# Performance work log

Measured on AMD Instinct MI355X. Metric: run time of the kernel, lower is better.

## Reference

```python
import jax, jax.numpy as jnp
from jax import lax
import numpy as np

L, D_LOCAL, BOND, BATCH = 64, 2, 64, 4096
STDDEV = 0.01  # default_kernel_init = normal(stddev=0.01)


def setup_inputs() -> dict:
    key = jax.random.key(0)
    k1, k2 = jax.random.split(key)
    x = jax.random.randint(k1, (BATCH, L), 0, D_LOCAL, dtype=jnp.int32)
    tensors_param = STDDEV * jax.random.normal(k2, (L, D_LOCAL, BOND, BOND), dtype=jnp.float32)
    return {"x": x, "tensors_param": tensors_param}


def reference(x, tensors_param):
    # tensors = param + identity (as in setup())
    P, d, D, _ = tensors_param.shape
    tensors = tensors_param + jnp.eye(D, dtype=tensors_param.dtype)  # [P, d, D, D]
    Lx = x.shape[-1]
    # tile unit cell across the chain (symperiod == L here, so tile factor is 1)
    all_tensors = jnp.tile(tensors, (Lx // P, 1, 1, 1))  # [L, d, D, D]
    B = x.shape[0]
    edge0 = jnp.broadcast_to(jnp.eye(D, dtype=tensors.dtype), (B, D, D))

    def step(edge, pair):
        t, qn = pair                      # t: [d, D, D], qn: [B]
        A = t[qn]                         # gather local matrices -> [B, D, D]
        return jnp.einsum('bij,bjk->bik', edge, A), None

    edge, _ = lax.scan(step, edge0, (all_tensors, x.T))  # scan over L sites
    psi = jnp.trace(edge, axis1=-2, axis2=-1)            # [B]
    return jnp.log(psi.astype(jnp.complex64))
```

## Files before the change

### kernel.cpp

```cpp
#include <hip/hip_runtime.h>


typedef __attribute__((ext_vector_type(8))) __bf16 bf16x8;
typedef __attribute__((ext_vector_type(4))) float f32x4;
typedef __attribute__((ext_vector_type(4))) int   int4v;

#define MFMA16(a, b, c) __builtin_amdgcn_mfma_f32_16x16x32_bf16((a), (b), (c), 0, 0, 0)

union frag_u { int4v i; bf16x8 v; };

__device__ __forceinline__ unsigned short f2bf(float f) {
  union { float f; unsigned u; } v; v.f = f;
  unsigned r = v.u + 0x7fffu + ((v.u >> 16) & 1u);
  return (unsigned short)(r >> 16);
}

__global__ __launch_bounds__(256) void prep_kernel(const float* __restrict__ p,
                                                   unsigned short* __restrict__ Tn,
                                                   unsigned short* __restrict__ Tt) {
  int t = blockIdx.x * 256 + threadIdx.x;
  int j  = t & 63;
  int i  = (t >> 6) & 63;
  int pq = t >> 12;
  float v = p[t] + ((i == j) ? 1.0f : 0.0f);
  unsigned short h = f2bf(v);
  Tn[t] = h;
  Tt[(((size_t)pq) << 12) + (size_t)j * 64 + i] = h;
}

__global__ __launch_bounds__(256) void build_p8_kernel(const unsigned short* __restrict__ Tn,
                                                       const unsigned short* __restrict__ Tt,
                                                       unsigned short* __restrict__ P8n,
                                                       unsigned short* __restrict__ P8t) {
  const int tid = threadIdx.x;
  const int l   = tid & 63;
  const int w   = blockIdx.x * 4 + (tid >> 6);
  const int s   = w >> 8, cmb = w & 255;
  const int c   = l & 15, p = l >> 4;

  const int srcA = (l & 15) | ((l & 16) << 1);
  const int srcB = srcA | 16;
  const bool hi5 = (l & 32) != 0;

  frag_u B[2][4];
  {
    int m7 = (8 * s + 7) * 2 + (cmb & 1);
    const unsigned short* base = Tt + ((size_t)m7 << 12);
#pragma unroll
    for (int ks = 0; ks < 2; ++ks)
#pragma unroll
      for (int nj = 0; nj < 4; ++nj)
        B[ks][nj].i = *reinterpret_cast<const int4v*>(base + (c + 16 * nj) * 64 + 32 * ks + 8 * p);
  }

#pragma unroll
  for (int j = 6; j >= 1; --j) {
    int m = (8 * s + j) * 2 + ((cmb >> (7 - j)) & 1);
    const unsigned short* abase = Tn + ((size_t)m << 12);
    frag_u A[4][2];
#pragma unroll
    for (int mi = 0; mi < 4; ++mi)
#pragma unroll
      for (int ks = 0; ks < 2; ++ks)
        A[mi][ks].i = *reinterpret_cast<const int4v*>(abase + (c + 16 * mi) * 64 + 32 * ks + 8 * p);

    int pk[4][4][2];
#pragma unroll
    for (int mi = 0; mi < 4; ++mi)
#pragma unroll
      for (int nj = 0; nj < 4; ++nj) {
        f32x4 d = {0.f, 0.f, 0.f, 0.f};
        d = MFMA16(A[mi][0].v, B[0][nj].v, d);
        d = MFMA16(A[mi][1].v, B[1][nj].v, d);
        asm("v_cvt_pk_bf16_f32 %0, %1, %2" : "=v"(pk[mi][nj][0]) : "v"(d[0]), "v"(d[1]));
        asm("v_cvt_pk_bf16_f32 %0, %1, %2" : "=v"(pk[mi][nj][1]) : "v"(d[2]), "v"(d[3]));
      }
#pragma unroll
    for (int ks = 0; ks < 2; ++ks)
#pragma unroll
      for (int nj = 0; nj < 4; ++nj) {
        int lo0 = pk[2 * ks][nj][0],     lo1 = pk[2 * ks][nj][1];
        int hi0 = pk[2 * ks + 1][nj][0], hi1 = pk[2 * ks + 1][nj][1];
        int a0 = __shfl(lo0, srcA, 64), b0 = __shfl(hi0, srcA, 64);
        int a1 = __shfl(lo1, srcA, 64), b1 = __shfl(hi1, srcA, 64);
        int a2 = __shfl(lo0, srcB, 64), b2 = __shfl(hi0, srcB, 64);
        int a3 = __shfl(lo1, srcB, 64), b3 = __shfl(hi1, srcB, 64);
        int4v nb = { hi5 ? b0 : a0, hi5 ? b1 : a1, hi5 ? b2 : a2, hi5 ? b3 : a3 };
        B[ks][nj].i = nb;
      }
  }

  {
    int m0 = (8 * s) * 2 + ((cmb >> 7) & 1);
    const unsigned short* abase = Tn + ((size_t)m0 << 12);
    frag_u A[4][2];
#pragma unroll
    for (int mi = 0; mi < 4; ++mi)
#pragma unroll
      for (int ks = 0; ks < 2; ++ks)
        A[mi][ks].i = *reinterpret_cast<const int4v*>(abase + (c + 16 * mi) * 64 + 32 * ks + 8 * p);

    unsigned short* ON = P8n + (((size_t)w) << 12);
    unsigned short* OT = P8t + (((size_t)w) << 12);
#pragma unroll
    for (int mi = 0; mi < 4; ++mi)
#pragma unroll
      for (int nj = 0; nj < 4; ++nj) {
        f32x4 d = {0.f, 0.f, 0.f, 0.f};
        d = MFMA16(A[mi][0].v, B[0][nj].v, d);
        d = MFMA16(A[mi][1].v, B[1][nj].v, d);
        if (s < 7) {
          int row0 = 16 * mi + 4 * p, col = 16 * nj + c;
#pragma unroll
          for (int r = 0; r < 4; ++r)
            ON[(size_t)(row0 + r) * 64 + col] = f2bf(d[r]);
        } else {
          int n = 16 * nj + c, m0r = 16 * mi + 4 * p;
          ushort4 pkv;
          pkv.x = f2bf(d[0]); pkv.y = f2bf(d[1]);
          pkv.z = f2bf(d[2]); pkv.w = f2bf(d[3]);
          *reinterpret_cast<ushort4*>(OT + (size_t)n * 64 + m0r) = pkv;
        }
      }
  }
}

__global__ __launch_bounds__(256) void chain_wave_kernel(const int* __restrict__ x,
                                                         const unsigned short* __restrict__ P8n,
                                                         const unsigned short* __restrict__ P8t,
                                                         float* __restrict__ out) {
  const int tid = threadIdx.x;
  const int l   = tid & 63;
  const int b   = blockIdx.x * 4 + (tid >> 6);
  const int c   = l & 15;
  const int p   = l >> 4;

  unsigned long long mask = __ballot((x[b * 64 + l] & 1) != 0);
  int idx[8];
#pragma unroll
  for (int s = 0; s < 8; ++s) {
    unsigned byte = (unsigned)((mask >> (8 * s)) & 0xFFull);
    idx[s] = (int)(__builtin_bitreverse32(byte) >> 24);
  }

  const int srcA = (l & 15) | ((l & 16) << 1);
  const int srcB = srcA | 16;
  const bool hi5 = (l & 32) != 0;

  frag_u B[2][4];
  {
    const unsigned short* base = P8t + (((size_t)(7 * 256 + idx[7])) << 12);
#pragma unroll
    for (int ks = 0; ks < 2; ++ks)
#pragma unroll
      for (int nj = 0; nj < 4; ++nj)
        B[ks][nj].i = *reinterpret_cast<const int4v*>(base + (c + 16 * nj) * 64 + 32 * ks + 8 * p);
  }

#pragma unroll
  for (int s = 6; s >= 1; --s) {
    const unsigned short* abase = P8n + (((size_t)(s * 256 + idx[s])) << 12);
    frag_u A[4][2];
#pragma unroll
    for (int mi = 0; mi < 4; ++mi)
#pragma unroll
      for (int ks = 0; ks < 2; ++ks)
        A[mi][ks].i = *reinterpret_cast<const int4v*>(abase + (c + 16 * mi) * 64 + 32 * ks + 8 * p);

    int pk[4][4][2];
#pragma unroll
    for (int mi = 0; mi < 4; ++mi)
#pragma unroll
      for (int nj = 0; nj < 4; ++nj) {
        f32x4 d = {0.f, 0.f, 0.f, 0.f};
        d = MFMA16(A[mi][0].v, B[0][nj].v, d);
        d = MFMA16(A[mi][1].v, B[1][nj].v, d);
        asm("v_cvt_pk_bf16_f32 %0, %1, %2" : "=v"(pk[mi][nj][0]) : "v"(d[0]), "v"(d[1]));
        asm("v_cvt_pk_bf16_f32 %0, %1, %2" : "=v"(pk[mi][nj][1]) : "v"(d[2]), "v"(d[3]));
      }
#pragma unroll
    for (int ks = 0; ks < 2; ++ks)
#pragma unroll
      for (int nj = 0; nj < 4; ++nj) {
        int lo0 = pk[2 * ks][nj][0],     lo1 = pk[2 * ks][nj][1];
        int hi0 = pk[2 * ks + 1][nj][0], hi1 = pk[2 * ks + 1][nj][1];
        int a0 = __shfl(lo0, srcA, 64), b0 = __shfl(hi0, srcA, 64);
        int a1 = __shfl(lo1, srcA, 64), b1 = __shfl(hi1, srcA, 64);
        int a2 = __shfl(lo0, srcB, 64), b2 = __shfl(hi0, srcB, 64);
        int a3 = __shfl(lo1, srcB, 64), b3 = __shfl(hi1, srcB, 64);
        int4v nb = { hi5 ? b0 : a0, hi5 ? b1 : a1, hi5 ? b2 : a2, hi5 ? b3 : a3 };
        B[ks][nj].i = nb;
      }
  }

  float psum = 0.f;
  {
    const unsigned short* abase = P8n + (((size_t)idx[0]) << 12);
#pragma unroll
    for (int t = 0; t < 4; ++t) {
      frag_u A0, A1;
      A0.i = *reinterpret_cast<const int4v*>(abase + (c + 16 * t) * 64 + 0  + 8 * p);
      A1.i = *reinterpret_cast<const int4v*>(abase + (c + 16 * t) * 64 + 32 + 8 * p);
      f32x4 d = {0.f, 0.f, 0.f, 0.f};
      d = MFMA16(A0.v, B[0][t].v, d);
      d = MFMA16(A1.v, B[1][t].v, d);
      if (p == (c >> 2)) {
#pragma unroll
        for (int r = 0; r < 4; ++r) psum += (r == (c & 3)) ? d[r] : 0.f;
      }
    }
  }
#pragma unroll
  for (int o = 32; o > 0; o >>= 1) psum += __shfl_down(psum, o, 64);
  if (l == 0) out[b] = logf(fabsf(psum));
}

extern "C" void kernel_launch(void* const* d_in, const int* in_sizes, int n_in,
                              void* d_out, int out_size, void* d_ws, size_t ws_size,
                              hipStream_t stream) {
  const int*   x     = (const int*)d_in[0];
  const float* param = (const float*)d_in[1];
  float* out = (float*)d_out;

  char* ws = (char*)d_ws;
  unsigned short* Tn  = (unsigned short*)(ws + (0ull  << 20));
  unsigned short* Tt  = (unsigned short*)(ws + (1ull  << 20));
  unsigned short* P8n = (unsigned short*)(ws + (8ull  << 20));
  unsigned short* P8t = (unsigned short*)(ws + (24ull << 20));

  prep_kernel<<<2048, 256, 0, stream>>>(param, Tn, Tt);
  build_p8_kernel<<<512, 256, 0, stream>>>(Tn, Tt, P8n, P8t);
  chain_wave_kernel<<<1024, 256, 0, stream>>>(x, P8n, P8t, out);
}
```

Measured before the change: 66.13 us.

## Split each batch chain across two waves and combine halves via shared memory

Each batch element's 8-segment product chain is now split between two wavefronts. One wave computes the left half (segments 0..3) and the other the right half (segments 4..7), each starting from a transposed segment-3 or segment-7 matrix. The left half's product is written to LDS, and after a block sync the right-half wave computes the trace. This halves the serial MFMA dependency chain per batch and doubles the wave count, at the cost of extra P8t writes for segment 3 in the build kernel, an LDS round trip, a __syncthreads, and one extra full 64x64 product.

```diff
diff --git a/kernel.cpp b/kernel.cpp
--- a/kernel.cpp
+++ b/kernel.cpp
@@ -102,19 +102,22 @@
 
     unsigned short* ON = P8n + (((size_t)w) << 12);
     unsigned short* OT = P8t + (((size_t)w) << 12);
-#pragma unroll
-    for (int mi = 0; mi < 4; ++mi)
-#pragma unroll
-      for (int nj = 0; nj < 4; ++nj) {
-        f32x4 d = {0.f, 0.f, 0.f, 0.f};
-        d = MFMA16(A[mi][0].v, B[0][nj].v, d);
-        d = MFMA16(A[mi][1].v, B[1][nj].v, d);
-        if (s < 7) {
+    const bool wantN = (s < 7);
+    const bool wantT = (s == 3) || (s == 7);
+#pragma unroll
+    for (int mi = 0; mi < 4; ++mi)
+#pragma unroll
+      for (int nj = 0; nj < 4; ++nj) {
+        f32x4 d = {0.f, 0.f, 0.f, 0.f};
+        d = MFMA16(A[mi][0].v, B[0][nj].v, d);
+        d = MFMA16(A[mi][1].v, B[1][nj].v, d);
+        if (wantN) {
           int row0 = 16 * mi + 4 * p, col = 16 * nj + c;
 #pragma unroll
           for (int r = 0; r < 4; ++r)
             ON[(size_t)(row0 + r) * 64 + col] = f2bf(d[r]);
-        } else {
+        }
+        if (wantT) {
           int n = 16 * nj + c, m0r = 16 * mi + 4 * p;
           ushort4 pkv;
           pkv.x = f2bf(d[0]); pkv.y = f2bf(d[1]);
@@ -125,15 +128,21 @@
   }
 }
 
-__global__ __launch_bounds__(256) void chain_wave_kernel(const int* __restrict__ x,
-                                                         const unsigned short* __restrict__ P8n,
-                                                         const unsigned short* __restrict__ P8t,
-                                                         float* __restrict__ out) {
+#define ELROW 72
+
+__global__ __launch_bounds__(256) void chain_split_kernel(const int* __restrict__ x,
+                                                          const unsigned short* __restrict__ P8n,
+                                                          const unsigned short* __restrict__ P8t,
+                                                          float* __restrict__ out) {
+  __shared__ __align__(16) unsigned short EL[2][64 * ELROW];
+
   const int tid = threadIdx.x;
   const int l   = tid & 63;
-  const int b   = blockIdx.x * 4 + (tid >> 6);
-  const int c   = l & 15;
-  const int p   = l >> 4;
+  const int w   = tid >> 6;
+  const int bl  = w >> 1;
+  const int h   = w & 1;
+  const int b   = blockIdx.x * 2 + bl;
+  const int c   = l & 15, p = l >> 4;
 
   unsigned long long mask = __ballot((x[b * 64 + l] & 1) != 0);
   int idx[8];
@@ -149,7 +158,8 @@
 
   frag_u B[2][4];
   {
-    const unsigned short* base = P8t + (((size_t)(7 * 256 + idx[7])) << 12);
+    const int sg = 4 * h + 3;
+    const unsigned short* base = P8t + (((size_t)(sg * 256 + idx[sg])) << 12);
 #pragma unroll
     for (int ks = 0; ks < 2; ++ks)
 #pragma unroll
@@ -157,8 +167,8 @@
         B[ks][nj].i = *reinterpret_cast<const int4v*>(base + (c + 16 * nj) * 64 + 32 * ks + 8 * p);
   }
 
-#pragma unroll
-  for (int s = 6; s >= 1; --s) {
+  for (int t = 0; t < 2 + h; ++t) {
+    const int s = 4 * h + 2 - t;
     const unsigned short* abase = P8n + (((size_t)(s * 256 + idx[s])) << 12);
     frag_u A[4][2];
 #pragma unroll
@@ -193,26 +203,47 @@
       }
   }
 
-  float psum = 0.f;
-  {
+  if (h == 0) {
     const unsigned short* abase = P8n + (((size_t)idx[0]) << 12);
-#pragma unroll
-    for (int t = 0; t < 4; ++t) {
+    frag_u A[4][2];
+#pragma unroll
+    for (int mi = 0; mi < 4; ++mi)
+#pragma unroll
+      for (int ks = 0; ks < 2; ++ks)
+        A[mi][ks].i = *reinterpret_cast<const int4v*>(abase + (c + 16 * mi) * 64 + 32 * ks + 8 * p);
+#pragma unroll
+    for (int mi = 0; mi < 4; ++mi)
+#pragma unroll
+      for (int nj = 0; nj < 4; ++nj) {
+        f32x4 d = {0.f, 0.f, 0.f, 0.f};
+        d = MFMA16(A[mi][0].v, B[0][nj].v, d);
+        d = MFMA16(A[mi][1].v, B[1][nj].v, d);
+        int row0 = 16 * mi + 4 * p, col = 16 * nj + c;
+#pragma unroll
+        for (int r = 0; r < 4; ++r)
+          EL[bl][(row0 + r) * ELROW + col] = f2bf(d[r]);
+      }
+  }
+  __syncthreads();
+  if (h == 1) {
+    float psum = 0.f;
+#pragma unroll
+    for (int t2 = 0; t2 < 4; ++t2) {
       frag_u A0, A1;
-      A0.i = *reinterpret_cast<const int4v*>(abase + (c + 16 * t) * 64 + 0  + 8 * p);
-      A1.i = *reinterpret_cast<const int4v*>(abase + (c + 16 * t) * 64 + 32 + 8 * p);
+      A0.i = *reinterpret_cast<const int4v*>(&EL[bl][(c + 16 * t2) * ELROW + 8 * p]);
+      A1.i = *reinterpret_cast<const int4v*>(&EL[bl][(c + 16 * t2) * ELROW + 32 + 8 * p]);
       f32x4 d = {0.f, 0.f, 0.f, 0.f};
-      d = MFMA16(A0.v, B[0][t].v, d);
-      d = MFMA16(A1.v, B[1][t].v, d);
+      d = MFMA16(A0.v, B[0][t2].v, d);
+      d = MFMA16(A1.v, B[1][t2].v, d);
       if (p == (c >> 2)) {
 #pragma unroll
         for (int r = 0; r < 4; ++r) psum += (r == (c & 3)) ? d[r] : 0.f;
       }
     }
-  }
-#pragma unroll
-  for (int o = 32; o > 0; o >>= 1) psum += __shfl_down(psum, o, 64);
-  if (l == 0) out[b] = logf(fabsf(psum));
+#pragma unroll
+    for (int o = 32; o > 0; o >>= 1) psum += __shfl_down(psum, o, 64);
+    if (l == 0) out[b] = logf(fabsf(psum));
+  }
 }
 
 extern "C" void kernel_launch(void* const* d_in, const int* in_sizes, int n_in,
@@ -230,5 +261,5 @@
 
   prep_kernel<<<2048, 256, 0, stream>>>(param, Tn, Tt);
   build_p8_kernel<<<512, 256, 0, stream>>>(Tn, Tt, P8n, P8t);
-  chain_wave_kernel<<<1024, 256, 0, stream>>>(x, P8n, P8t, out);
-}
+  chain_split_kernel<<<2048, 256, 0, stream>>>(x, P8n, P8t, out);
+}
```

Measured after the change: 69.71 us. 1.05x slower.

## Precompute 4-site products instead of 8-site products for the chain contraction

Applied to the files above, without the earlier changes.

Shrinks the precomputed product table from all 256 combinations of 8 consecutive sites to all 16 combinations of 4 sites. Table construction work drops from 2048 products of 8 matrices to 256 products of 4, and the table becomes small enough to stay in cache. In exchange, the per-sample chain kernel now performs 16 matrix multiplies per sample instead of 8, and its main loop is no longer unrolled. This trades per-sample compute for much cheaper setup and lower memory traffic.

```diff
diff --git a/kernel.cpp b/kernel.cpp
--- a/kernel.cpp
+++ b/kernel.cpp
@@ -28,14 +28,14 @@
   Tt[(((size_t)pq) << 12) + (size_t)j * 64 + i] = h;
 }
 
-__global__ __launch_bounds__(256) void build_p8_kernel(const unsigned short* __restrict__ Tn,
+__global__ __launch_bounds__(256) void build_p4_kernel(const unsigned short* __restrict__ Tn,
                                                        const unsigned short* __restrict__ Tt,
-                                                       unsigned short* __restrict__ P8n,
-                                                       unsigned short* __restrict__ P8t) {
+                                                       unsigned short* __restrict__ P4n,
+                                                       unsigned short* __restrict__ P4t) {
   const int tid = threadIdx.x;
   const int l   = tid & 63;
   const int w   = blockIdx.x * 4 + (tid >> 6);
-  const int s   = w >> 8, cmb = w & 255;
+  const int s   = w >> 4, cmb = w & 15;
   const int c   = l & 15, p = l >> 4;
 
   const int srcA = (l & 15) | ((l & 16) << 1);
@@ -44,8 +44,8 @@
 
   frag_u B[2][4];
   {
-    int m7 = (8 * s + 7) * 2 + (cmb & 1);
-    const unsigned short* base = Tt + ((size_t)m7 << 12);
+    int m3 = (4 * s + 3) * 2 + (cmb & 1);
+    const unsigned short* base = Tt + ((size_t)m3 << 12);
 #pragma unroll
     for (int ks = 0; ks < 2; ++ks)
 #pragma unroll
@@ -54,8 +54,8 @@
   }
 
 #pragma unroll
-  for (int j = 6; j >= 1; --j) {
-    int m = (8 * s + j) * 2 + ((cmb >> (7 - j)) & 1);
+  for (int j = 2; j >= 1; --j) {
+    int m = (4 * s + j) * 2 + ((cmb >> (3 - j)) & 1);
     const unsigned short* abase = Tn + ((size_t)m << 12);
     frag_u A[4][2];
 #pragma unroll
@@ -91,7 +91,7 @@
   }
 
   {
-    int m0 = (8 * s) * 2 + ((cmb >> 7) & 1);
+    int m0 = (4 * s) * 2 + ((cmb >> 3) & 1);
     const unsigned short* abase = Tn + ((size_t)m0 << 12);
     frag_u A[4][2];
 #pragma unroll
@@ -100,8 +100,9 @@
       for (int ks = 0; ks < 2; ++ks)
         A[mi][ks].i = *reinterpret_cast<const int4v*>(abase + (c + 16 * mi) * 64 + 32 * ks + 8 * p);
 
-    unsigned short* ON = P8n + (((size_t)w) << 12);
-    unsigned short* OT = P8t + (((size_t)w) << 12);
+    unsigned short* ON = P4n + (((size_t)w) << 12);
+    unsigned short* OT = P4t + (((size_t)cmb) << 12);
+    const bool wantT = (s == 15);
 #pragma unroll
     for (int mi = 0; mi < 4; ++mi)
 #pragma unroll
@@ -109,12 +110,11 @@
         f32x4 d = {0.f, 0.f, 0.f, 0.f};
         d = MFMA16(A[mi][0].v, B[0][nj].v, d);
         d = MFMA16(A[mi][1].v, B[1][nj].v, d);
-        if (s < 7) {
-          int row0 = 16 * mi + 4 * p, col = 16 * nj + c;
-#pragma unroll
-          for (int r = 0; r < 4; ++r)
-            ON[(size_t)(row0 + r) * 64 + col] = f2bf(d[r]);
-        } else {
+        int row0 = 16 * mi + 4 * p, col = 16 * nj + c;
+#pragma unroll
+        for (int r = 0; r < 4; ++r)
+          ON[(size_t)(row0 + r) * 64 + col] = f2bf(d[r]);
+        if (wantT) {
           int n = 16 * nj + c, m0r = 16 * mi + 4 * p;
           ushort4 pkv;
           pkv.x = f2bf(d[0]); pkv.y = f2bf(d[1]);
@@ -126,8 +126,8 @@
 }
 
 __global__ __launch_bounds__(256) void chain_wave_kernel(const int* __restrict__ x,
-                                                         const unsigned short* __restrict__ P8n,
-                                                         const unsigned short* __restrict__ P8t,
+                                                         const unsigned short* __restrict__ P4n,
+                                                         const unsigned short* __restrict__ P4t,
                                                          float* __restrict__ out) {
   const int tid = threadIdx.x;
   const int l   = tid & 63;
@@ -136,11 +136,11 @@
   const int p   = l >> 4;
 
   unsigned long long mask = __ballot((x[b * 64 + l] & 1) != 0);
-  int idx[8];
-#pragma unroll
-  for (int s = 0; s < 8; ++s) {
-    unsigned byte = (unsigned)((mask >> (8 * s)) & 0xFFull);
-    idx[s] = (int)(__builtin_bitreverse32(byte) >> 24);
+  int idx[16];
+#pragma unroll
+  for (int s = 0; s < 16; ++s) {
+    unsigned nib = (unsigned)((mask >> (4 * s)) & 0xFull);
+    idx[s] = (int)(__builtin_bitreverse32(nib) >> 28);
   }
 
   const int srcA = (l & 15) | ((l & 16) << 1);
@@ -149,7 +149,7 @@
 
   frag_u B[2][4];
   {
-    const unsigned short* base = P8t + (((size_t)(7 * 256 + idx[7])) << 12);
+    const unsigned short* base = P4t + (((size_t)idx[15]) << 12);
 #pragma unroll
     for (int ks = 0; ks < 2; ++ks)
 #pragma unroll
@@ -157,9 +157,8 @@
         B[ks][nj].i = *reinterpret_cast<const int4v*>(base + (c + 16 * nj) * 64 + 32 * ks + 8 * p);
   }
 
-#pragma unroll
-  for (int s = 6; s >= 1; --s) {
-    const unsigned short* abase = P8n + (((size_t)(s * 256 + idx[s])) << 12);
+  for (int s = 14; s >= 1; --s) {
+    const unsigned short* abase = P4n + (((size_t)(s * 16 + idx[s])) << 12);
     frag_u A[4][2];
 #pragma unroll
     for (int mi = 0; mi < 4; ++mi)
@@ -195,7 +194,7 @@
 
   float psum = 0.f;
   {
-    const unsigned short* abase = P8n + (((size_t)idx[0]) << 12);
+    const unsigned short* abase = P4n + (((size_t)idx[0]) << 12);
 #pragma unroll
     for (int t = 0; t < 4; ++t) {
       frag_u A0, A1;
@@ -223,12 +222,12 @@
   float* out = (float*)d_out;
 
   char* ws = (char*)d_ws;
-  unsigned short* Tn  = (unsigned short*)(ws + (0ull  << 20));
-  unsigned short* Tt  = (unsigned short*)(ws + (1ull  << 20));
-  unsigned short* P8n = (unsigned short*)(ws + (8ull  << 20));
-  unsigned short* P8t = (unsigned short*)(ws + (24ull << 20));
+  unsigned short* Tn  = (unsigned short*)(ws + (0ull << 20));
+  unsigned short* Tt  = (unsigned short*)(ws + (1ull << 20));
+  unsigned short* P4n = (unsigned short*)(ws + (2ull << 20));
+  unsigned short* P4t = (unsigned short*)(ws + (4ull << 20));
 
   prep_kernel<<<2048, 256, 0, stream>>>(param, Tn, Tt);
-  build_p8_kernel<<<512, 256, 0, stream>>>(Tn, Tt, P8n, P8t);
-  chain_wave_kernel<<<1024, 256, 0, stream>>>(x, P8n, P8t, out);
-}
+  build_p4_kernel<<<64, 256, 0, stream>>>(Tn, Tt, P4n, P4t);
+  chain_wave_kernel<<<1024, 256, 0, stream>>>(x, P4n, P4t, out);
+}
```

New measurement: 82.35 us. 24.5% more time.
